# Optimization experiments

Hardware: AMD Instinct MI355X
Metric: run time of the kernel (lower is better)

## Reference

```python
import jax, jax.numpy as jnp
import numpy as np

N = 1024
IN_FEATURES = 128
N_HEADS = 8
N_HIDDEN = 16  # out_features // n_heads = 128 // 8
NEG_SLOPE = 0.2


def setup_inputs() -> dict:
    key = jax.random.key(0)
    k1, k2, k3, k4, k5 = jax.random.split(key, 5)
    h = jax.random.normal(k1, (N, IN_FEATURES), dtype=jnp.float32)
    adj_mat = jax.random.randint(k2, (N, N, 1), 0, 2, dtype=jnp.int32)
    s = jax.random.normal(k3, (N, N, 1), dtype=jnp.float32)
    # linear: nn.Linear(in_features, n_hidden*n_heads, bias=False) -> weight [128, 128]
    W = jax.random.normal(k4, (N_HEADS * N_HIDDEN, IN_FEATURES), dtype=jnp.float32) * 0.1
    # attn: nn.Linear(2*n_hidden, 1, bias=False) -> weight [1, 32]; stored flat [32]
    attn_w = jax.random.normal(k5, (2 * N_HIDDEN,), dtype=jnp.float32) * 0.1
    return {"h": h, "adj_mat": adj_mat, "s": s, "W": W, "attn_w": attn_w}


def reference(h, adj_mat, s, W, attn_w):
    n_nodes = h.shape[0]
    # g: [N, heads, hidden]
    g = (h @ W.T).reshape(n_nodes, N_HEADS, N_HIDDEN)
    # attn(cat(g_i, g_j)) = a_src . g_i + a_dst . g_j  (linear decomposes over concat)
    a_src = attn_w[:N_HIDDEN]
    a_dst = attn_w[N_HIDDEN:]
    src = jnp.einsum('ihf,f->ih', g, a_src)  # [N, heads]
    dst = jnp.einsum('jhf,f->jh', g, a_dst)  # [N, heads]
    e = jax.nn.leaky_relu(src[:, None, :] + dst[None, :, :], NEG_SLOPE)  # [N, N, heads]
    mask = adj_mat == 0  # [N, N, 1] broadcasts over heads
    neg_inf = jnp.array(-jnp.inf, dtype=e.dtype)
    e = jnp.where(mask, neg_inf, e)
    s_masked = jnp.where(mask, neg_inf, s)  # [N, N, 1]
    a = jax.nn.softmax(e, axis=1)               # [N, N, heads]
    s_prime = jax.nn.softmax(s_masked, axis=1)  # [N, N, 1]
    # NOTE: original applies a third softmax to (a + s_prime) WITHOUT re-masking,
    # so non-edge entries (value 0) get nonzero weight exp(0)/Z — replicated faithfully.
    new_attention = jax.nn.softmax(a + s_prime, axis=1)  # [N, N, heads]
    # dropout is identity in eval mode
    attn_res = jnp.einsum('ijh,jhf->ihf', new_attention, g)  # [N, heads, hidden]
    return attn_res.reshape(n_nodes, N_HEADS * N_HIDDEN)
```

## Files before the change

kernel.cpp:

```cpp
#include <hip/hip_runtime.h>

#define NNODES 1024
#define NHEADS 8
#define NHID 16
#define DIM 128
#define NEG_SLOPE 0.2f

__global__ __launch_bounds__(128) void proj_kernel(
    const float* __restrict__ h, const float* __restrict__ W,
    const float* __restrict__ attn_w,
    float* __restrict__ g, float* __restrict__ srcv, float* __restrict__ dstv)
{
    const int i = blockIdx.x;
    const int o = threadIdx.x;
    __shared__ float hs[DIM];
    hs[o] = h[(size_t)i * DIM + o];
    __syncthreads();
    const float4* hv = (const float4*)hs;
    const float4* wv = (const float4*)(W + (size_t)o * DIM);
    float acc = 0.f;
#pragma unroll
    for (int k = 0; k < DIM / 4; k++) {
        float4 a = hv[k]; float4 b = wv[k];
        acc = fmaf(a.x, b.x, fmaf(a.y, b.y, fmaf(a.z, b.z, fmaf(a.w, b.w, acc))));
    }
    g[(size_t)i * DIM + o] = acc;
    const int f  = o & (NHID - 1);
    const int hd = o >> 4;
    float sv = acc * attn_w[f];
    float dv = acc * attn_w[NHID + f];
#pragma unroll
    for (int off = 8; off > 0; off >>= 1) {
        sv += __shfl_xor(sv, off, 64);
        dv += __shfl_xor(dv, off, 64);
    }
    if (f == 0) { srcv[i * NHEADS + hd] = sv; dstv[i * NHEADS + hd] = dv; }
}

__global__ __launch_bounds__(256, 2) void fused_kernel(
    const int* __restrict__ adj, const float* __restrict__ s,
    const float* __restrict__ g, const float* __restrict__ srcv,
    const float* __restrict__ dstv, float* __restrict__ out)
{
    const int i0   = blockIdx.x * 2;
    const int tid  = threadIdx.x;
    const int h    = tid & 7;
    const int js   = tid >> 3;
    const int lane = tid & 63;
    const int wv   = tid >> 6;

    __shared__ float evL[2][NNODES];
    __shared__ float zeA[4][NHEADS][2];
    __shared__ float zsA[4][2];
    __shared__ float statE[2][NHEADS];
    __shared__ float statS[2];
    __shared__ float redO[4][2][NHEADS][16];
    __shared__ float ztA[4][2][NHEADS];

    float zs[2] = {0.f, 0.f};
#pragma unroll
    for (int r = 0; r < 2; r++) {
        const int4   a  = ((const int4*)  adj)[(size_t)(i0 + r) * (NNODES/4) + tid];
        const float4 sv = ((const float4*)s  )[(size_t)(i0 + r) * (NNODES/4) + tid];
        float4 e4;
        e4.x = a.x ? __expf(sv.x) : 0.f;
        e4.y = a.y ? __expf(sv.y) : 0.f;
        e4.z = a.z ? __expf(sv.z) : 0.f;
        e4.w = a.w ? __expf(sv.w) : 0.f;
        ((float4*)evL[r])[tid] = e4;
        zs[r] += e4.x + e4.y + e4.z + e4.w;
    }
    const float sH[2] = { srcv[(size_t)i0 * NHEADS + h],
                          srcv[(size_t)(i0 + 1) * NHEADS + h] };
    __syncthreads();

    float ze[2] = {0.f, 0.f};
#pragma unroll 4
    for (int t = 0; t < 32; t++) {
        const int j = t * 32 + js;
        const float d = dstv[j * NHEADS + h];
#pragma unroll
        for (int r = 0; r < 2; r++) {
            float e = sH[r] + d;
            e = e > 0.f ? e : NEG_SLOPE * e;
            const float x = __expf(e);
            ze[r] += (evL[r][j] != 0.f) ? x : 0.f;
        }
    }
#pragma unroll
    for (int off = 8; off <= 32; off <<= 1)
#pragma unroll
        for (int r = 0; r < 2; r++) ze[r] += __shfl_xor(ze[r], off, 64);
#pragma unroll
    for (int off = 1; off <= 32; off <<= 1)
#pragma unroll
        for (int r = 0; r < 2; r++) zs[r] += __shfl_xor(zs[r], off, 64);
    if (lane < NHEADS) { zeA[wv][lane][0] = ze[0]; zeA[wv][lane][1] = ze[1]; }
    if (lane == 0)     { zsA[wv][0] = zs[0]; zsA[wv][1] = zs[1]; }
    __syncthreads();
    if (tid < 16) {
        const int hh = tid & 7, rr = tid >> 3;
        statE[rr][hh] = 1.f / (zeA[0][hh][rr] + zeA[1][hh][rr] +
                               zeA[2][hh][rr] + zeA[3][hh][rr]);
    } else if (tid < 18) {
        const int rr = tid - 16;
        statS[rr] = 1.f / (zsA[0][rr] + zsA[1][rr] + zsA[2][rr] + zsA[3][rr]);
    }
    __syncthreads();
    const float ize[2] = { statE[0][h], statE[1][h] };
    const float izs[2] = { statS[0],    statS[1]    };

    float acc[2][16];
#pragma unroll
    for (int r = 0; r < 2; r++)
#pragma unroll
        for (int f = 0; f < 16; f++) acc[r][f] = 0.f;
    float zt[2] = {0.f, 0.f};

#pragma unroll 2
    for (int t = 0; t < 32; t++) {
        const int j = t * 32 + js;
        const float d = dstv[j * NHEADS + h];
        const float4* gj = (const float4*)(g + (size_t)j * DIM + h * NHID);
        const float4 g0 = gj[0], g1 = gj[1], g2 = gj[2], g3 = gj[3];
#pragma unroll
        for (int r = 0; r < 2; r++) {
            const float ev = evL[r][j];
            float e = sH[r] + d;
            e = e > 0.f ? e : NEG_SLOPE * e;
            const float w = (ev != 0.f)
                ? __expf(__expf(e) * ize[r] + ev * izs[r])
                : 1.0f;
            zt[r] += w;
            acc[r][0]  = fmaf(w, g0.x, acc[r][0]);
            acc[r][1]  = fmaf(w, g0.y, acc[r][1]);
            acc[r][2]  = fmaf(w, g0.z, acc[r][2]);
            acc[r][3]  = fmaf(w, g0.w, acc[r][3]);
            acc[r][4]  = fmaf(w, g1.x, acc[r][4]);
            acc[r][5]  = fmaf(w, g1.y, acc[r][5]);
            acc[r][6]  = fmaf(w, g1.z, acc[r][6]);
            acc[r][7]  = fmaf(w, g1.w, acc[r][7]);
            acc[r][8]  = fmaf(w, g2.x, acc[r][8]);
            acc[r][9]  = fmaf(w, g2.y, acc[r][9]);
            acc[r][10] = fmaf(w, g2.z, acc[r][10]);
            acc[r][11] = fmaf(w, g2.w, acc[r][11]);
            acc[r][12] = fmaf(w, g3.x, acc[r][12]);
            acc[r][13] = fmaf(w, g3.y, acc[r][13]);
            acc[r][14] = fmaf(w, g3.z, acc[r][14]);
            acc[r][15] = fmaf(w, g3.w, acc[r][15]);
        }
    }

#pragma unroll
    for (int off = 8; off <= 32; off <<= 1)
#pragma unroll
        for (int r = 0; r < 2; r++) {
#pragma unroll
            for (int f = 0; f < 16; f++)
                acc[r][f] += __shfl_xor(acc[r][f], off, 64);
            zt[r] += __shfl_xor(zt[r], off, 64);
        }
    if (lane < NHEADS) {
#pragma unroll
        for (int r = 0; r < 2; r++) {
#pragma unroll
            for (int f = 0; f < 16; f++) redO[wv][r][lane][f] = acc[r][f];
            ztA[wv][r][lane] = zt[r];
        }
    }
    __syncthreads();
    {
        const int rr = tid >> 7;
        const int hf = tid & 127;
        const int oh = hf >> 4;
        const int f  = hf & 15;
        const float v  = redO[0][rr][oh][f] + redO[1][rr][oh][f] +
                         redO[2][rr][oh][f] + redO[3][rr][oh][f];
        const float zq = ztA[0][rr][oh] + ztA[1][rr][oh] +
                         ztA[2][rr][oh] + ztA[3][rr][oh];
        out[(size_t)(i0 + rr) * DIM + hf] = v / zq;
    }
}

extern "C" void kernel_launch(void* const* d_in, const int* in_sizes, int n_in,
                              void* d_out, int out_size, void* d_ws, size_t ws_size,
                              hipStream_t stream) {
    const float* h      = (const float*)d_in[0];
    const int*   adj    = (const int*)  d_in[1];
    const float* s      = (const float*)d_in[2];
    const float* W      = (const float*)d_in[3];
    const float* attn_w = (const float*)d_in[4];
    float* out = (float*)d_out;

    float* g    = (float*)d_ws;
    float* srcv = g    + (size_t)NNODES * DIM;
    float* dstv = srcv + (size_t)NNODES * NHEADS;

    proj_kernel <<<NNODES, DIM, 0, stream>>>(h, W, attn_w, g, srcv, dstv);
    fused_kernel<<<NNODES / 2, 256, 0, stream>>>(adj, s, g, srcv, dstv, out);
}
```

Baseline: 95.50 us.

## Split fused kernel blocks across head halves to double grid size

Each block now covers two rows and only four of the eight heads, so the grid grows from 512 to 1024 blocks and the launch bound asks for four blocks per SM instead of two. Each thread covers four times fewer heads per j-sweep but more j values, and the shuffle reductions start at offset 4. The cost is that the adjacency and s rows are loaded and exponentiated twice, once per head half, adding redundant memory traffic. The weight expression is also rewritten so a single exp runs with a masked argument instead of a branch.

```diff
diff --git a/kernel.cpp b/kernel.cpp
--- a/kernel.cpp
+++ b/kernel.cpp
@@ -37,25 +37,28 @@
     if (f == 0) { srcv[i * NHEADS + hd] = sv; dstv[i * NHEADS + hd] = dv; }
 }
 
-__global__ __launch_bounds__(256, 2) void fused_kernel(
+__global__ __launch_bounds__(256, 4) void fused_kernel(
     const int* __restrict__ adj, const float* __restrict__ s,
     const float* __restrict__ g, const float* __restrict__ srcv,
     const float* __restrict__ dstv, float* __restrict__ out)
 {
-    const int i0   = blockIdx.x * 2;
+    const int rp   = blockIdx.x >> 1;
+    const int hh   = blockIdx.x & 1;
+    const int i0   = rp * 2;
     const int tid  = threadIdx.x;
-    const int h    = tid & 7;
-    const int js   = tid >> 3;
+    const int h4   = tid & 3;
+    const int h    = hh * 4 + h4;
+    const int js   = tid >> 2;
     const int lane = tid & 63;
     const int wv   = tid >> 6;
 
     __shared__ float evL[2][NNODES];
-    __shared__ float zeA[4][NHEADS][2];
+    __shared__ float zeA[4][4][2];
     __shared__ float zsA[4][2];
-    __shared__ float statE[2][NHEADS];
+    __shared__ float statE[2][4];
     __shared__ float statS[2];
-    __shared__ float redO[4][2][NHEADS][16];
-    __shared__ float ztA[4][2][NHEADS];
+    __shared__ float redO[4][2][4][16];
+    __shared__ float ztA[4][2][4];
 
     float zs[2] = {0.f, 0.f};
 #pragma unroll
@@ -76,8 +79,8 @@
 
     float ze[2] = {0.f, 0.f};
 #pragma unroll 4
-    for (int t = 0; t < 32; t++) {
-        const int j = t * 32 + js;
+    for (int t = 0; t < 16; t++) {
+        const int j = t * 64 + js;
         const float d = dstv[j * NHEADS + h];
 #pragma unroll
         for (int r = 0; r < 2; r++) {
@@ -88,27 +91,27 @@
         }
     }
 #pragma unroll
-    for (int off = 8; off <= 32; off <<= 1)
+    for (int off = 4; off <= 32; off <<= 1)
 #pragma unroll
         for (int r = 0; r < 2; r++) ze[r] += __shfl_xor(ze[r], off, 64);
 #pragma unroll
     for (int off = 1; off <= 32; off <<= 1)
 #pragma unroll
         for (int r = 0; r < 2; r++) zs[r] += __shfl_xor(zs[r], off, 64);
-    if (lane < NHEADS) { zeA[wv][lane][0] = ze[0]; zeA[wv][lane][1] = ze[1]; }
-    if (lane == 0)     { zsA[wv][0] = zs[0]; zsA[wv][1] = zs[1]; }
-    __syncthreads();
-    if (tid < 16) {
-        const int hh = tid & 7, rr = tid >> 3;
-        statE[rr][hh] = 1.f / (zeA[0][hh][rr] + zeA[1][hh][rr] +
-                               zeA[2][hh][rr] + zeA[3][hh][rr]);
-    } else if (tid < 18) {
-        const int rr = tid - 16;
+    if (lane < 4)  { zeA[wv][lane][0] = ze[0]; zeA[wv][lane][1] = ze[1]; }
+    if (lane == 0) { zsA[wv][0] = zs[0]; zsA[wv][1] = zs[1]; }
+    __syncthreads();
+    if (tid < 8) {
+        const int hq = tid & 3, rr = tid >> 2;
+        statE[rr][hq] = 1.f / (zeA[0][hq][rr] + zeA[1][hq][rr] +
+                               zeA[2][hq][rr] + zeA[3][hq][rr]);
+    } else if (tid < 10) {
+        const int rr = tid - 8;
         statS[rr] = 1.f / (zsA[0][rr] + zsA[1][rr] + zsA[2][rr] + zsA[3][rr]);
     }
     __syncthreads();
-    const float ize[2] = { statE[0][h], statE[1][h] };
-    const float izs[2] = { statS[0],    statS[1]    };
+    const float ize[2] = { statE[0][h4], statE[1][h4] };
+    const float izs[2] = { statS[0],     statS[1]     };
 
     float acc[2][16];
 #pragma unroll
@@ -118,8 +121,8 @@
     float zt[2] = {0.f, 0.f};
 
 #pragma unroll 2
-    for (int t = 0; t < 32; t++) {
-        const int j = t * 32 + js;
+    for (int t = 0; t < 16; t++) {
+        const int j = t * 64 + js;
         const float d = dstv[j * NHEADS + h];
         const float4* gj = (const float4*)(g + (size_t)j * DIM + h * NHID);
         const float4 g0 = gj[0], g1 = gj[1], g2 = gj[2], g3 = gj[3];
@@ -128,9 +131,9 @@
             const float ev = evL[r][j];
             float e = sH[r] + d;
             e = e > 0.f ? e : NEG_SLOPE * e;
-            const float w = (ev != 0.f)
-                ? __expf(__expf(e) * ize[r] + ev * izs[r])
-                : 1.0f;
+            const float x   = __expf(e);
+            const float arg = (ev != 0.f) ? fmaf(x, ize[r], ev * izs[r]) : 0.f;
+            const float w   = __expf(arg);
             zt[r] += w;
             acc[r][0]  = fmaf(w, g0.x, acc[r][0]);
             acc[r][1]  = fmaf(w, g0.y, acc[r][1]);
@@ -152,7 +155,7 @@
     }
 
 #pragma unroll
-    for (int off = 8; off <= 32; off <<= 1)
+    for (int off = 4; off <= 32; off <<= 1)
 #pragma unroll
         for (int r = 0; r < 2; r++) {
 #pragma unroll
@@ -160,7 +163,7 @@
                 acc[r][f] += __shfl_xor(acc[r][f], off, 64);
             zt[r] += __shfl_xor(zt[r], off, 64);
         }
-    if (lane < NHEADS) {
+    if (lane < 4) {
 #pragma unroll
         for (int r = 0; r < 2; r++) {
 #pragma unroll
@@ -169,16 +172,16 @@
         }
     }
     __syncthreads();
-    {
-        const int rr = tid >> 7;
-        const int hf = tid & 127;
-        const int oh = hf >> 4;
-        const int f  = hf & 15;
+    if (tid < 128) {
+        const int rr = tid >> 6;
+        const int q  = tid & 63;
+        const int oh = q >> 4;
+        const int f  = q & 15;
         const float v  = redO[0][rr][oh][f] + redO[1][rr][oh][f] +
                          redO[2][rr][oh][f] + redO[3][rr][oh][f];
         const float zq = ztA[0][rr][oh] + ztA[1][rr][oh] +
                          ztA[2][rr][oh] + ztA[3][rr][oh];
-        out[(size_t)(i0 + rr) * DIM + hf] = v / zq;
+        out[(size_t)(i0 + rr) * DIM + hh * 64 + q] = v / zq;
     }
 }
 
@@ -197,5 +200,5 @@
     float* dstv = srcv + (size_t)NNODES * NHEADS;
 
     proj_kernel <<<NNODES, DIM, 0, stream>>>(h, W, attn_w, g, srcv, dstv);
-    fused_kernel<<<NNODES / 2, 256, 0, stream>>>(adj, s, g, srcv, dstv, out);
+    fused_kernel<<<NNODES, 256, 0, stream>>>(adj, s, g, srcv, dstv, out);
 }
```

Result: slower. 100.8 us (+5.5%).

## Fuse projection and attention into one cooperative kernel with grid sync

Applied to the files above, without the earlier changes.

Merges the projection kernel into the attention kernel. Each block computes g and the src/dst scores for its two rows, then a cooperative grid-wide sync makes all dst values and g visible before the attention pass. src scores stay in shared memory instead of going through global memory. The cost removed is the second kernel launch and its launch gap. In exchange it needs a cooperative launch, where all 512 blocks must be co-resident, and pays for a grid barrier. The softmax weight is also restructured so a single branch-free exp covers both the edge and non-edge cases.

```diff
diff --git a/kernel.cpp b/kernel.cpp
--- a/kernel.cpp
+++ b/kernel.cpp
@@ -1,4 +1,7 @@
 #include <hip/hip_runtime.h>
+#include <hip/hip_cooperative_groups.h>
+
+namespace cg = cooperative_groups;
 
 #define NNODES 1024
 #define NHEADS 8
@@ -6,49 +9,20 @@
 #define DIM 128
 #define NEG_SLOPE 0.2f
 
-__global__ __launch_bounds__(128) void proj_kernel(
-    const float* __restrict__ h, const float* __restrict__ W,
+__global__ __launch_bounds__(256, 2) void gat_kernel(
+    const float* __restrict__ hfeat, const int* __restrict__ adj,
+    const float* __restrict__ s, const float* __restrict__ W,
     const float* __restrict__ attn_w,
-    float* __restrict__ g, float* __restrict__ srcv, float* __restrict__ dstv)
-{
-    const int i = blockIdx.x;
-    const int o = threadIdx.x;
-    __shared__ float hs[DIM];
-    hs[o] = h[(size_t)i * DIM + o];
-    __syncthreads();
-    const float4* hv = (const float4*)hs;
-    const float4* wv = (const float4*)(W + (size_t)o * DIM);
-    float acc = 0.f;
-#pragma unroll
-    for (int k = 0; k < DIM / 4; k++) {
-        float4 a = hv[k]; float4 b = wv[k];
-        acc = fmaf(a.x, b.x, fmaf(a.y, b.y, fmaf(a.z, b.z, fmaf(a.w, b.w, acc))));
-    }
-    g[(size_t)i * DIM + o] = acc;
-    const int f  = o & (NHID - 1);
-    const int hd = o >> 4;
-    float sv = acc * attn_w[f];
-    float dv = acc * attn_w[NHID + f];
-#pragma unroll
-    for (int off = 8; off > 0; off >>= 1) {
-        sv += __shfl_xor(sv, off, 64);
-        dv += __shfl_xor(dv, off, 64);
-    }
-    if (f == 0) { srcv[i * NHEADS + hd] = sv; dstv[i * NHEADS + hd] = dv; }
-}
-
-__global__ __launch_bounds__(256, 2) void fused_kernel(
-    const int* __restrict__ adj, const float* __restrict__ s,
-    const float* __restrict__ g, const float* __restrict__ srcv,
-    const float* __restrict__ dstv, float* __restrict__ out)
+    float* __restrict__ g, float* __restrict__ dstv,
+    float* __restrict__ out)
 {
     const int i0   = blockIdx.x * 2;
     const int tid  = threadIdx.x;
-    const int h    = tid & 7;
-    const int js   = tid >> 3;
     const int lane = tid & 63;
     const int wv   = tid >> 6;
 
+    __shared__ float hs[2][DIM];
+    __shared__ float sh_src[2][NHEADS];
     __shared__ float evL[2][NNODES];
     __shared__ float zeA[4][NHEADS][2];
     __shared__ float zsA[4][2];
@@ -56,6 +30,40 @@
     __shared__ float statS[2];
     __shared__ float redO[4][2][NHEADS][16];
     __shared__ float ztA[4][2][NHEADS];
+
+    {
+        const int r1 = tid >> 7;
+        const int o  = tid & 127;
+        hs[r1][o] = hfeat[(size_t)(i0 + r1) * DIM + o];
+        __syncthreads();
+        const float4* hv = (const float4*)hs[r1];
+        const float4* wrow = (const float4*)(W + (size_t)o * DIM);
+        float acc = 0.f;
+#pragma unroll
+        for (int k = 0; k < DIM / 4; k++) {
+            float4 a = hv[k]; float4 b = wrow[k];
+            acc = fmaf(a.x, b.x, fmaf(a.y, b.y, fmaf(a.z, b.z, fmaf(a.w, b.w, acc))));
+        }
+        g[(size_t)(i0 + r1) * DIM + o] = acc;
+        const int f  = o & (NHID - 1);
+        const int hd = o >> 4;
+        float sv = acc * attn_w[f];
+        float dv = acc * attn_w[NHID + f];
+#pragma unroll
+        for (int off = 8; off > 0; off >>= 1) {
+            sv += __shfl_xor(sv, off, 64);
+            dv += __shfl_xor(dv, off, 64);
+        }
+        if (f == 0) {
+            sh_src[r1][hd] = sv;
+            dstv[(size_t)(i0 + r1) * NHEADS + hd] = dv;
+        }
+    }
+
+    cg::this_grid().sync();
+
+    const int h  = tid & 7;
+    const int js = tid >> 3;
 
     float zs[2] = {0.f, 0.f};
 #pragma unroll
@@ -70,8 +78,7 @@
         ((float4*)evL[r])[tid] = e4;
         zs[r] += e4.x + e4.y + e4.z + e4.w;
     }
-    const float sH[2] = { srcv[(size_t)i0 * NHEADS + h],
-                          srcv[(size_t)(i0 + 1) * NHEADS + h] };
+    const float sH[2] = { sh_src[0][h], sh_src[1][h] };
     __syncthreads();
 
     float ze[2] = {0.f, 0.f};
@@ -128,9 +135,9 @@
             const float ev = evL[r][j];
             float e = sH[r] + d;
             e = e > 0.f ? e : NEG_SLOPE * e;
-            const float w = (ev != 0.f)
-                ? __expf(__expf(e) * ize[r] + ev * izs[r])
-                : 1.0f;
+            const float x   = __expf(e);
+            const float arg = (ev != 0.f) ? fmaf(x, ize[r], ev * izs[r]) : 0.f;
+            const float w   = __expf(arg);
             zt[r] += w;
             acc[r][0]  = fmaf(w, g0.x, acc[r][0]);
             acc[r][1]  = fmaf(w, g0.y, acc[r][1]);
@@ -185,17 +192,17 @@
 extern "C" void kernel_launch(void* const* d_in, const int* in_sizes, int n_in,
                               void* d_out, int out_size, void* d_ws, size_t ws_size,
                               hipStream_t stream) {
-    const float* h      = (const float*)d_in[0];
+    const float* hfeat  = (const float*)d_in[0];
     const int*   adj    = (const int*)  d_in[1];
     const float* s      = (const float*)d_in[2];
     const float* W      = (const float*)d_in[3];
     const float* attn_w = (const float*)d_in[4];
-    float* out = (float*)d_out;
-
+    float* out  = (float*)d_out;
     float* g    = (float*)d_ws;
-    float* srcv = g    + (size_t)NNODES * DIM;
-    float* dstv = srcv + (size_t)NNODES * NHEADS;
-
-    proj_kernel <<<NNODES, DIM, 0, stream>>>(h, W, attn_w, g, srcv, dstv);
-    fused_kernel<<<NNODES / 2, 256, 0, stream>>>(adj, s, g, srcv, dstv, out);
+    float* dstv = g + (size_t)NNODES * DIM;
+
+    void* args[] = { (void*)&hfeat, (void*)&adj, (void*)&s, (void*)&W,
+                     (void*)&attn_w, (void*)&g, (void*)&dstv, (void*)&out };
+    hipLaunchCooperativeKernel((const void*)gat_kernel,
+                               dim3(NNODES / 2), dim3(256), args, 0, stream);
 }
```

New measurement: 158.0 us. +65.5%, slower.

## Stage dst scores in LDS and split feature dim across lane quads with shuffled weights

Applied to the files above, without the earlier changes.

Copies the full dstv array (32KB) into shared memory at block start so both passes read destination scores from LDS. The aggregation pass is remapped so each group of 4 lanes splits one head's 16 features (one float4 per lane): each lane computes a weight for one j and the weights are broadcast via shuffles. This cuts accumulator registers from 32 to 8 and shrinks the cross-lane reduction at the end. In exchange it adds per-block copies of dstv, extra shuffles per j, and more LDS use that may limit occupancy.

```diff
diff --git a/kernel.cpp b/kernel.cpp
--- a/kernel.cpp
+++ b/kernel.cpp
@@ -44,17 +44,22 @@
 {
     const int i0   = blockIdx.x * 2;
     const int tid  = threadIdx.x;
-    const int h    = tid & 7;
-    const int js   = tid >> 3;
     const int lane = tid & 63;
     const int wv   = tid >> 6;
+    const int hA   = tid & 7;
+    const int jsA  = tid >> 3;
+    const int qB   = tid & 3;
+    const int hB   = (tid >> 2) & 7;
+    const int jsB  = tid >> 5;
 
     __shared__ float evL[2][NNODES];
+    __shared__ float dstL[NNODES * NHEADS];
+    __shared__ float sh_src[2][NHEADS];
     __shared__ float zeA[4][NHEADS][2];
     __shared__ float zsA[4][2];
     __shared__ float statE[2][NHEADS];
     __shared__ float statS[2];
-    __shared__ float redO[4][2][NHEADS][16];
+    __shared__ float redO[4][2][NHEADS][4][4];
     __shared__ float ztA[4][2][NHEADS];
 
     float zs[2] = {0.f, 0.f};
@@ -70,21 +75,30 @@
         ((float4*)evL[r])[tid] = e4;
         zs[r] += e4.x + e4.y + e4.z + e4.w;
     }
-    const float sH[2] = { srcv[(size_t)i0 * NHEADS + h],
-                          srcv[(size_t)(i0 + 1) * NHEADS + h] };
+    {
+        const float4* dv4 = (const float4*)dstv;
+        float4* dl4 = (float4*)dstL;
+#pragma unroll
+        for (int k = 0; k < 8; k++) dl4[k * 256 + tid] = dv4[k * 256 + tid];
+        if (tid < 16) sh_src[tid >> 3][tid & 7] =
+            srcv[(size_t)(i0 + (tid >> 3)) * NHEADS + (tid & 7)];
+    }
     __syncthreads();
 
     float ze[2] = {0.f, 0.f};
+    {
+        const float sHA[2] = { sh_src[0][hA], sh_src[1][hA] };
 #pragma unroll 4
-    for (int t = 0; t < 32; t++) {
-        const int j = t * 32 + js;
-        const float d = dstv[j * NHEADS + h];
-#pragma unroll
-        for (int r = 0; r < 2; r++) {
-            float e = sH[r] + d;
-            e = e > 0.f ? e : NEG_SLOPE * e;
-            const float x = __expf(e);
-            ze[r] += (evL[r][j] != 0.f) ? x : 0.f;
+        for (int t = 0; t < 32; t++) {
+            const int j = t * 32 + jsA;
+            const float d = dstL[j * NHEADS + hA];
+#pragma unroll
+            for (int r = 0; r < 2; r++) {
+                float e = sHA[r] + d;
+                e = e > 0.f ? e : NEG_SLOPE * e;
+                const float x = __expf(e);
+                ze[r] += (evL[r][j] != 0.f) ? x : 0.f;
+            }
         }
     }
 #pragma unroll
@@ -107,75 +121,74 @@
         statS[rr] = 1.f / (zsA[0][rr] + zsA[1][rr] + zsA[2][rr] + zsA[3][rr]);
     }
     __syncthreads();
-    const float ize[2] = { statE[0][h], statE[1][h] };
-    const float izs[2] = { statS[0],    statS[1]    };
-
-    float acc[2][16];
+
+    const float ize[2] = { statE[0][hB], statE[1][hB] };
+    const float izs[2] = { statS[0],     statS[1]     };
+    const float sHB[2] = { sh_src[0][hB], sh_src[1][hB] };
+    const int   base   = lane & ~3;
+
+    float acc[2][4] = {{0.f,0.f,0.f,0.f},{0.f,0.f,0.f,0.f}};
+    float zt[2] = {0.f, 0.f};
+    const float4* g4 = (const float4*)g;
+
+#pragma unroll 2
+    for (int tg = 0; tg < 32; tg++) {
+        const int jw = (tg * 4 + qB) * 8 + jsB;
+        const float d = dstL[jw * NHEADS + hB];
+        float w[2];
+#pragma unroll
+        for (int r = 0; r < 2; r++) {
+            float e = sHB[r] + d;
+            e = e > 0.f ? e : NEG_SLOPE * e;
+            const float x  = __expf(e);
+            const float ev = evL[r][jw];
+            const float arg = (ev != 0.f) ? fmaf(x, ize[r], ev * izs[r]) : 0.f;
+            w[r] = __expf(arg);
+            zt[r] += w[r];
+        }
+#pragma unroll
+        for (int k = 0; k < 4; k++) {
+            const int j = (tg * 4 + k) * 8 + jsB;
+            const float4 gv = g4[(size_t)j * 32 + hB * 4 + qB];
+            const float w0 = __shfl(w[0], base + k, 64);
+            const float w1 = __shfl(w[1], base + k, 64);
+            acc[0][0] = fmaf(w0, gv.x, acc[0][0]);
+            acc[0][1] = fmaf(w0, gv.y, acc[0][1]);
+            acc[0][2] = fmaf(w0, gv.z, acc[0][2]);
+            acc[0][3] = fmaf(w0, gv.w, acc[0][3]);
+            acc[1][0] = fmaf(w1, gv.x, acc[1][0]);
+            acc[1][1] = fmaf(w1, gv.y, acc[1][1]);
+            acc[1][2] = fmaf(w1, gv.z, acc[1][2]);
+            acc[1][3] = fmaf(w1, gv.w, acc[1][3]);
+        }
+    }
+
 #pragma unroll
     for (int r = 0; r < 2; r++)
 #pragma unroll
-        for (int f = 0; f < 16; f++) acc[r][f] = 0.f;
-    float zt[2] = {0.f, 0.f};
-
-#pragma unroll 2
-    for (int t = 0; t < 32; t++) {
-        const int j = t * 32 + js;
-        const float d = dstv[j * NHEADS + h];
-        const float4* gj = (const float4*)(g + (size_t)j * DIM + h * NHID);
-        const float4 g0 = gj[0], g1 = gj[1], g2 = gj[2], g3 = gj[3];
-#pragma unroll
-        for (int r = 0; r < 2; r++) {
-            const float ev = evL[r][j];
-            float e = sH[r] + d;
-            e = e > 0.f ? e : NEG_SLOPE * e;
-            const float w = (ev != 0.f)
-                ? __expf(__expf(e) * ize[r] + ev * izs[r])
-                : 1.0f;
-            zt[r] += w;
-            acc[r][0]  = fmaf(w, g0.x, acc[r][0]);
-            acc[r][1]  = fmaf(w, g0.y, acc[r][1]);
-            acc[r][2]  = fmaf(w, g0.z, acc[r][2]);
-            acc[r][3]  = fmaf(w, g0.w, acc[r][3]);
-            acc[r][4]  = fmaf(w, g1.x, acc[r][4]);
-            acc[r][5]  = fmaf(w, g1.y, acc[r][5]);
-            acc[r][6]  = fmaf(w, g1.z, acc[r][6]);
-            acc[r][7]  = fmaf(w, g1.w, acc[r][7]);
-            acc[r][8]  = fmaf(w, g2.x, acc[r][8]);
-            acc[r][9]  = fmaf(w, g2.y, acc[r][9]);
-            acc[r][10] = fmaf(w, g2.z, acc[r][10]);
-            acc[r][11] = fmaf(w, g2.w, acc[r][11]);
-            acc[r][12] = fmaf(w, g3.x, acc[r][12]);
-            acc[r][13] = fmaf(w, g3.y, acc[r][13]);
-            acc[r][14] = fmaf(w, g3.z, acc[r][14]);
-            acc[r][15] = fmaf(w, g3.w, acc[r][15]);
-        }
-    }
-
-#pragma unroll
-    for (int off = 8; off <= 32; off <<= 1)
-#pragma unroll
-        for (int r = 0; r < 2; r++) {
-#pragma unroll
-            for (int f = 0; f < 16; f++)
-                acc[r][f] += __shfl_xor(acc[r][f], off, 64);
-            zt[r] += __shfl_xor(zt[r], off, 64);
-        }
-    if (lane < NHEADS) {
-#pragma unroll
-        for (int r = 0; r < 2; r++) {
-#pragma unroll
-            for (int f = 0; f < 16; f++) redO[wv][r][lane][f] = acc[r][f];
-            ztA[wv][r][lane] = zt[r];
-        }
+        for (int m = 0; m < 4; m++) acc[r][m] += __shfl_xor(acc[r][m], 32, 64);
+#pragma unroll
+    for (int r = 0; r < 2; r++) {
+        zt[r] += __shfl_xor(zt[r], 1, 64);
+        zt[r] += __shfl_xor(zt[r], 2, 64);
+        zt[r] += __shfl_xor(zt[r], 32, 64);
+    }
+    if (lane < 32) {
+#pragma unroll
+        for (int r = 0; r < 2; r++)
+            *(float4*)&redO[wv][r][hB][qB][0] =
+                make_float4(acc[r][0], acc[r][1], acc[r][2], acc[r][3]);
+        if ((lane & 3) == 0) { ztA[wv][0][hB] = zt[0]; ztA[wv][1][hB] = zt[1]; }
     }
     __syncthreads();
     {
         const int rr = tid >> 7;
         const int hf = tid & 127;
         const int oh = hf >> 4;
-        const int f  = hf & 15;
-        const float v  = redO[0][rr][oh][f] + redO[1][rr][oh][f] +
-                         redO[2][rr][oh][f] + redO[3][rr][oh][f];
+        const int qq = (hf >> 2) & 3;
+        const int mm = hf & 3;
+        const float v  = redO[0][rr][oh][qq][mm] + redO[1][rr][oh][qq][mm] +
+                         redO[2][rr][oh][qq][mm] + redO[3][rr][oh][qq][mm];
         const float zq = ztA[0][rr][oh] + ztA[1][rr][oh] +
                          ztA[2][rr][oh] + ztA[3][rr][oh];
         out[(size_t)(i0 + rr) * DIM + hf] = v / zq;
```

Result: faster. 87.43 us (-8.4%).
